# Performance work log

Measured on AMD Instinct MI355X. Metric: run time of the kernel, lower is better.

## Reference

```python
import jax, jax.numpy as jnp
import numpy as np

FLOW_ITERS = 8
DUAL_ITERS = 8
DUAL_STEP = 0.1
DUAL_MOM = 0.9
GRAPH_LAYERS = 2
BIG = 1e9


def _sparsemax(z, mask):
    # sparsemax along last axis; masked entries already hold -BIG, zeroed by mask after.
    V = z.shape[-1]
    zs = jnp.sort(z, axis=-1)[..., ::-1]
    cum = jnp.cumsum(zs, axis=-1)
    k = jnp.arange(1, V + 1, dtype=z.dtype)
    support = zs * k > (cum - 1.0)
    k_sel = jnp.sum(support.astype(jnp.int32), axis=-1, keepdims=True)
    tau = (jnp.take_along_axis(cum, k_sel - 1, axis=-1) - 1.0) / k_sel.astype(z.dtype)
    return jnp.maximum(z - tau, 0.0) * mask


def _min_cost_flow(props, demands):
    # iterative proportional flow routing: push relu(inflow - demand) along predicted proportions
    def body(flow, _):
        inflow = jnp.sum(flow, axis=1)[..., None]      # [B,V,1] inflow to each node
        adjusted = jax.nn.relu(inflow - demands)       # excess to re-route
        return props * adjusted, None                  # row i scaled by its excess
    flow0 = jnp.zeros_like(props)
    flow, _ = jax.lax.scan(body, flow0, None, length=FLOW_ITERS)
    return flow


def _dual_flow(dual_diff, adj):
    # Nesterov-momentum projected gradient on cost(x)=x^2 minus linear dual term, x>=0 on edges
    def body(carry, _):
        flow, acc = carry
        look = flow - DUAL_MOM * acc
        grad = 2.0 * look - dual_diff                  # d/dx x^2 - dual_diff
        acc = DUAL_MOM * acc + DUAL_STEP * grad
        flow = adj * jax.nn.relu(flow - acc)
        return (flow, acc), None
    z = jnp.zeros_like(dual_diff)
    (flow, _), _ = jax.lax.scan(body, (z, z), None, length=DUAL_ITERS)
    return flow


def setup_inputs():
    key = jax.random.key(0)
    ks = jax.random.split(key, 32)
    B, V, F, E, D, K, H = 8, 1200, 8, 16, 64, 2, 4
    node_features = jax.random.normal(ks[0], (B, V, F), dtype=jnp.float32)
    node_embeddings = jax.random.normal(ks[1], (B, V, E), dtype=jnp.float32)
    d = jax.random.normal(ks[2], (B, V, 1), dtype=jnp.float32)
    demands = d - jnp.mean(d, axis=1, keepdims=True)   # balanced supply/demand per graph
    eye = jnp.eye(V, dtype=jnp.float32)
    adj = (jax.random.uniform(ks[3], (B, V, V)) < (16.0 / V)).astype(jnp.float32) * (1.0 - eye)
    hop2 = jnp.clip(adj @ adj, 0.0, 1.0) * (1.0 - eye)
    neighborhoods = jnp.stack([adj, hop2], axis=0)     # [K,B,V,V] k-hop neighborhoods

    def dense(k, fin, fout):
        return (jax.random.normal(k, (fin, fout), dtype=jnp.float32) / np.sqrt(fin)).astype(jnp.float32)

    return dict(
        node_features=node_features, node_embeddings=node_embeddings,
        demands=demands, adj=adj, neighborhoods=neighborhoods,
        enc_w0=dense(ks[4], E + F, D), enc_b0=jnp.zeros((D,), jnp.float32),
        enc_w1=dense(ks[5], D, D), enc_b1=jnp.zeros((D,), jnp.float32),
        agg_w=(jax.random.normal(ks[6], (K, D, D)) / np.sqrt(D)).astype(jnp.float32),
        agg_b=jnp.zeros((K, D), jnp.float32),
        att_w=(jax.random.normal(ks[7], (H, D, D)) / np.sqrt(D)).astype(jnp.float32),
        att_b=jnp.zeros((H, D), jnp.float32),
        att_v=(jax.random.normal(ks[8], (H, D)) / np.sqrt(D)).astype(jnp.float32),
        gru_wu=dense(ks[9], 2 * D, D), gru_bu=jnp.zeros((D,), jnp.float32),
        gru_wr=dense(ks[10], 2 * D, D), gru_br=jnp.zeros((D,), jnp.float32),
        gru_wc=dense(ks[11], 2 * D, D), gru_bc=jnp.zeros((D,), jnp.float32),
        dec_w0=dense(ks[12], D, D), dec_b0=jnp.zeros((D,), jnp.float32),
        dec_w1=dense(ks[13], D, 1), dec_b1=jnp.zeros((1,), jnp.float32),
        dual_w0=dense(ks[14], D, D), dual_b0=jnp.zeros((D,), jnp.float32),
        dual_w1=dense(ks[15], D, 1), dual_b1=jnp.zeros((1,), jnp.float32),
    )


def reference(node_features, node_embeddings, demands, adj, neighborhoods,
              enc_w0, enc_b0, enc_w1, enc_b1, agg_w, agg_b, att_w, att_b, att_v,
              gru_wu, gru_bu, gru_wr, gru_br, gru_wc, gru_bc,
              dec_w0, dec_b0, dec_w1, dec_b1, dual_w0, dual_b0, dual_w1, dual_b1):
    H = att_w.shape[0]
    # node encoder MLP (tanh hidden, tanh final since activate_final=True)
    x = jnp.concatenate([node_embeddings, node_features], axis=-1)
    enc = jnp.tanh(jnp.tanh(x @ enc_w0 + enc_b0) @ enc_w1 + enc_b1)            # [B,V,D]

    deg = jnp.sum(neighborhoods, axis=-1, keepdims=True)
    nb_norm = neighborhoods / jnp.maximum(deg, 1.0)                            # [K,B,V,V]

    for _ in range(GRAPH_LAYERS):
        # per-hop neighborhood aggregation
        msg = jnp.einsum('kbuv,bvd->kbud', nb_norm, enc)
        agg = jnp.tanh(jnp.einsum('kbud,kde->kbue', msg, agg_w) + agg_b[:, None, None, :])
        # multi-head attention over the K hop levels
        proj = jnp.tanh(jnp.einsum('kbvd,hde->hkbve', agg, att_w) + att_b[:, None, None, None, :])
        scores = jnp.einsum('hkbve,he->hkbv', proj, att_v)
        attn = jax.nn.softmax(scores, axis=1)                                  # softmax over hops
        nxt = jnp.einsum('hkbv,kbvd->bvd', attn, agg) / H                      # mean over heads
        # GRU state update
        xs = jnp.concatenate([nxt, enc], axis=-1)
        u = jax.nn.sigmoid(xs @ gru_wu + gru_bu)
        r = jax.nn.sigmoid(xs @ gru_wr + gru_br)
        c = jnp.tanh(jnp.concatenate([nxt, r * enc], axis=-1) @ gru_wc + gru_bc)
        enc = u * enc + (1.0 - u) * c

    # primal: edge weights -> sparsemax -> min-cost-flow
    pred = (enc @ dec_w0 + dec_b0) @ dec_w1 + dec_b1                           # [B,V,1]
    pred_weights = adj * jnp.transpose(pred, (0, 2, 1))                        # [B,V,V]
    weights = -BIG * (1.0 - adj) + pred_weights
    flow_props = _sparsemax(weights, adj)
    flow = _min_cost_flow(flow_props, demands)
    flow_cost = jnp.sum(flow * flow, axis=(1, 2))                              # square cost

    # dual: potentials -> dual-diff -> dual flow solver
    dual = (enc @ dual_w0 + dual_b0) @ dual_w1 + dual_b1                       # [B,V,1]
    dual_diff = adj * (dual - jnp.transpose(dual, (0, 2, 1)))
    dflow = _dual_flow(dual_diff, adj)
    dual_demand = jnp.sum(dual * demands, axis=(1, 2))
    dual_cost = jnp.sum(dflow * dflow - dual_diff * dflow, axis=(1, 2)) - dual_demand

    return flow_cost - dual_cost                                               # duality-gap loss, [B]
```

## Files before the change

kernel.cpp:

```cpp
#include <hip/hip_runtime.h>

#define BB 8
#define VV 1200
#define DD 64
#define KH 2
#define NH 4
#define CAP 64
#define NB2CAP 384
#define NROW (BB*VV)
#define NKROW (KH*BB*VV)

__device__ __forceinline__ float wredsum(float v) {
#pragma unroll
  for (int o = 32; o > 0; o >>= 1) v += __shfl_xor(v, o, 64);
  return v;
}
__device__ __forceinline__ float gredsum(float v) {
#pragma unroll
  for (int o = 8; o > 0; o >>= 1) v += __shfl_xor(v, o, 64);
  return v;
}

__device__ __forceinline__ float tanh_f(float x) {
  float e = __expf(2.0f * x);
  return 1.0f - 2.0f / (e + 1.0f);
}
__device__ __forceinline__ float sigmoid_f(float x) { return 1.0f / (1.0f + __expf(-x)); }

__device__ __forceinline__ unsigned pack_bf16x2(float a, float b) {
  unsigned ua = __float_as_uint(a), ub = __float_as_uint(b);
  ua = (ua + 0x7fffu + ((ua >> 16) & 1u)) >> 16;
  ub = (ub + 0x7fffu + ((ub >> 16) & 1u)) & 0xffff0000u;
  return ua | ub;
}
__device__ __forceinline__ float bf_lo(unsigned u) { return __uint_as_float(u << 16); }
__device__ __forceinline__ float bf_hi(unsigned u) { return __uint_as_float(u & 0xffff0000u); }

__device__ __forceinline__ size_t nb_base(int row) {
  return (row < NROW) ? (size_t)row * CAP
                      : (size_t)NROW * CAP + (size_t)(row - NROW) * NB2CAP;
}

#define ENC2B (NROW / 64)
#define CSR2B (NKROW / 8)
__global__ void __launch_bounds__(512) k_pre(
    const float* __restrict__ nb, int* __restrict__ nb_cols, int* __restrict__ nb_cnt,
    const float* __restrict__ emb, const float* __restrict__ feat,
    const float* __restrict__ w0, const float* __restrict__ b0,
    const float* __restrict__ w1, const float* __restrict__ b1,
    unsigned* __restrict__ enc0,
    int* __restrict__ col_cnt, float* __restrict__ out, int out_size) {
  __shared__ float Xe[64][25];
  __shared__ float Ht[64][65];
  int bid = blockIdx.x;
  int tid = threadIdx.x;
  if (bid < ENC2B) {
    int tile0 = bid * 64;
    if (tid < 256) {
      int i = tid >> 2, f = tid & 3;
      float4 e4 = *(const float4*)(emb + (size_t)(tile0 + i) * 16 + f * 4);
      Xe[i][f * 4] = e4.x; Xe[i][f * 4 + 1] = e4.y; Xe[i][f * 4 + 2] = e4.z; Xe[i][f * 4 + 3] = e4.w;
    } else if (tid < 384) {
      int t = tid - 256; int i = t >> 1, f = t & 1;
      float4 f4 = *(const float4*)(feat + (size_t)(tile0 + i) * 8 + f * 4);
      Xe[i][16 + f * 4] = f4.x; Xe[i][16 + f * 4 + 1] = f4.y;
      Xe[i][16 + f * 4 + 2] = f4.z; Xe[i][16 + f * 4 + 3] = f4.w;
    }
    __syncthreads();
    int rsub = tid >> 4, cg = tid & 15;
    int c0 = cg * 4, r0 = rsub * 2;
    float a[2][4];
#pragma unroll
    for (int i = 0; i < 2; ++i)
#pragma unroll
      for (int j = 0; j < 4; ++j) a[i][j] = b0[c0 + j];
#pragma unroll
    for (int kk = 0; kk < 24; ++kk) {
      float4 w4 = *(const float4*)(w0 + kk * DD + c0);
      float x0 = Xe[r0][kk], x1 = Xe[r0 + 1][kk];
      a[0][0] = fmaf(x0, w4.x, a[0][0]); a[0][1] = fmaf(x0, w4.y, a[0][1]);
      a[0][2] = fmaf(x0, w4.z, a[0][2]); a[0][3] = fmaf(x0, w4.w, a[0][3]);
      a[1][0] = fmaf(x1, w4.x, a[1][0]); a[1][1] = fmaf(x1, w4.y, a[1][1]);
      a[1][2] = fmaf(x1, w4.z, a[1][2]); a[1][3] = fmaf(x1, w4.w, a[1][3]);
    }
#pragma unroll
    for (int i = 0; i < 2; ++i) {
      Ht[r0 + i][c0] = tanh_f(a[i][0]); Ht[r0 + i][c0 + 1] = tanh_f(a[i][1]);
      Ht[r0 + i][c0 + 2] = tanh_f(a[i][2]); Ht[r0 + i][c0 + 3] = tanh_f(a[i][3]);
    }
    __syncthreads();
    float g[2][4];
#pragma unroll
    for (int i = 0; i < 2; ++i)
#pragma unroll
      for (int j = 0; j < 4; ++j) g[i][j] = b1[c0 + j];
#pragma unroll 8
    for (int kk = 0; kk < DD; ++kk) {
      float4 w4 = *(const float4*)(w1 + kk * DD + c0);
      float x0 = Ht[r0][kk], x1 = Ht[r0 + 1][kk];
      g[0][0] = fmaf(x0, w4.x, g[0][0]); g[0][1] = fmaf(x0, w4.y, g[0][1]);
      g[0][2] = fmaf(x0, w4.z, g[0][2]); g[0][3] = fmaf(x0, w4.w, g[0][3]);
      g[1][0] = fmaf(x1, w4.x, g[1][0]); g[1][1] = fmaf(x1, w4.y, g[1][1]);
      g[1][2] = fmaf(x1, w4.z, g[1][2]); g[1][3] = fmaf(x1, w4.w, g[1][3]);
    }
#pragma unroll
    for (int i = 0; i < 2; ++i) {
      uint2 pk;
      pk.x = pack_bf16x2(tanh_f(g[i][0]), tanh_f(g[i][1]));
      pk.y = pack_bf16x2(tanh_f(g[i][2]), tanh_f(g[i][3]));
      ((uint2*)enc0)[(size_t)(tile0 + r0 + i) * 16 + cg] = pk;
    }
  } else if (bid < ENC2B + CSR2B) {
    int w = tid >> 6, lane = tid & 63;
    int row = (bid - ENC2B) * 8 + w;
    const float4* nb4 = (const float4*)(nb + (size_t)row * VV);
    float4 v[5];
#pragma unroll
    for (int c = 0; c < 4; ++c) v[c] = nb4[c * 64 + lane];
    v[4].x = v[4].y = v[4].z = v[4].w = 0.0f;
    if (lane < 44) v[4] = nb4[256 + lane];
    unsigned long long ltmask = (lane == 0) ? 0ull : ((1ull << lane) - 1ull);
    size_t base = nb_base(row);
    int cap = (row < NROW) ? CAP : NB2CAP;
    int off_base = 0;
#pragma unroll
    for (int c = 0; c < 5; ++c) {
      int nz0 = (v[c].x != 0.0f), nz1 = (v[c].y != 0.0f);
      int nz2 = (v[c].z != 0.0f), nz3 = (v[c].w != 0.0f);
      unsigned long long m0 = __ballot(nz0 != 0);
      unsigned long long m1 = __ballot(nz1 != 0);
      unsigned long long m2 = __ballot(nz2 != 0);
      unsigned long long m3 = __ballot(nz3 != 0);
      int lanepref = __popcll(m0 & ltmask) + __popcll(m1 & ltmask)
                   + __popcll(m2 & ltmask) + __popcll(m3 & ltmask);
      int chunkcnt = __popcll(m0) + __popcll(m1) + __popcll(m2) + __popcll(m3);
      int off = off_base + lanepref;
      int vi = (c * 64 + lane) * 4;
      if (nz0 && off < cap) nb_cols[base + off] = vi;
      off += nz0;
      if (nz1 && off < cap) nb_cols[base + off] = vi + 1;
      off += nz1;
      if (nz2 && off < cap) nb_cols[base + off] = vi + 2;
      off += nz2;
      if (nz3 && off < cap) nb_cols[base + off] = vi + 3;
      off_base += chunkcnt;
    }
    if (lane == 0) nb_cnt[row] = (off_base > cap) ? cap : off_base;
  } else {
    for (int i = tid; i < NROW; i += 512) col_cnt[i] = 0;
    if (tid < out_size) out[tid] = 0.0f;
  }
}

__global__ void __launch_bounds__(256) k_aggatt(
    const int* __restrict__ nb_cols, const int* __restrict__ nb_cnt,
    const unsigned* __restrict__ encIn,
    const float* __restrict__ agg_w, const float* __restrict__ agg_b,
    const float* __restrict__ att_w, const float* __restrict__ att_b,
    const float* __restrict__ att_v,
    float* __restrict__ agg, float* __restrict__ scores) {
  __shared__ float M[16][65];
  __shared__ float G[16][65];
  int tid = threadIdx.x;
  int tile0 = blockIdx.x * 16;
  int k = (tile0 >= NROW) ? 1 : 0;
  int bv0 = tile0 - k * NROW;
  int wid = tid >> 6, lane = tid & 63;
  int sub = lane >> 4, q = lane & 15;
  for (int ii = 0; ii < 4; ++ii) {
    int i = wid * 4 + ii;
    int row = tile0 + i;
    int bv = row - k * NROW;
    int b = bv / VV;
    const uint2* encU = (const uint2*)(encIn + (size_t)b * VV * 32);
    const int* cols = nb_cols + nb_base(row);
    int n = nb_cnt[row];
    float ax = 0.0f, ay = 0.0f, az = 0.0f, aw = 0.0f;
    int j = 0;
    int cc0 = 0, cc1 = 0, cc2 = 0, cc3 = 0;
    if (j + 16 <= n) {
      cc0 = cols[j + sub]; cc1 = cols[j + 4 + sub];
      cc2 = cols[j + 8 + sub]; cc3 = cols[j + 12 + sub];
    }
    while (j + 16 <= n) {
      int nj = j + 16;
      int p0 = 0, p1 = 0, p2 = 0, p3 = 0;
      if (nj + 16 <= n) {
        p0 = cols[nj + sub]; p1 = cols[nj + 4 + sub];
        p2 = cols[nj + 8 + sub]; p3 = cols[nj + 12 + sub];
      }
      uint2 u0 = encU[(size_t)cc0 * 16 + q];
      uint2 u1 = encU[(size_t)cc1 * 16 + q];
      uint2 u2 = encU[(size_t)cc2 * 16 + q];
      uint2 u3 = encU[(size_t)cc3 * 16 + q];
      ax += (bf_lo(u0.x) + bf_lo(u1.x)) + (bf_lo(u2.x) + bf_lo(u3.x));
      ay += (bf_hi(u0.x) + bf_hi(u1.x)) + (bf_hi(u2.x) + bf_hi(u3.x));
      az += (bf_lo(u0.y) + bf_lo(u1.y)) + (bf_lo(u2.y) + bf_lo(u3.y));
      aw += (bf_hi(u0.y) + bf_hi(u1.y)) + (bf_hi(u2.y) + bf_hi(u3.y));
      cc0 = p0; cc1 = p1; cc2 = p2; cc3 = p3;
      j = nj;
    }
    for (; j < n; j += 4) {
      int idx = j + sub;
      if (idx < n) {
        uint2 u = encU[(size_t)cols[idx] * 16 + q];
        ax += bf_lo(u.x); ay += bf_hi(u.x); az += bf_lo(u.y); aw += bf_hi(u.y);
      }
    }
#pragma unroll
    for (int o = 16; o < 64; o <<= 1) {
      ax += __shfl_xor(ax, o, 64);
      ay += __shfl_xor(ay, o, 64);
      az += __shfl_xor(az, o, 64);
      aw += __shfl_xor(aw, o, 64);
    }
    if (lane < 16) {
      float inv = 1.0f / fmaxf((float)n, 1.0f);
      M[i][q * 4] = ax * inv; M[i][q * 4 + 1] = ay * inv;
      M[i][q * 4 + 2] = az * inv; M[i][q * 4 + 3] = aw * inv;
    }
  }
  __syncthreads();
  int r = tid >> 4, cg = tid & 15;
  int c0 = cg * 4;
  const float* W = agg_w + (size_t)k * DD * DD;
  float acc[4];
#pragma unroll
  for (int j = 0; j < 4; ++j) acc[j] = agg_b[k * DD + c0 + j];
#pragma unroll 8
  for (int kk = 0; kk < DD; ++kk) {
    float4 w4 = *(const float4*)(W + kk * DD + c0);
    float x0 = M[r][kk];
    acc[0] = fmaf(x0, w4.x, acc[0]); acc[1] = fmaf(x0, w4.y, acc[1]);
    acc[2] = fmaf(x0, w4.z, acc[2]); acc[3] = fmaf(x0, w4.w, acc[3]);
  }
  float4 g4;
  g4.x = tanh_f(acc[0]); g4.y = tanh_f(acc[1]);
  g4.z = tanh_f(acc[2]); g4.w = tanh_f(acc[3]);
  G[r][c0] = g4.x; G[r][c0 + 1] = g4.y; G[r][c0 + 2] = g4.z; G[r][c0 + 3] = g4.w;
  *(float4*)(agg + (size_t)(tile0 + r) * DD + c0) = g4;
  __syncthreads();
#pragma unroll
  for (int h = 0; h < NH; ++h) {
    const float* Wh = att_w + (size_t)h * DD * DD;
    float a2[4];
#pragma unroll
    for (int j = 0; j < 4; ++j) a2[j] = att_b[h * DD + c0 + j];
#pragma unroll 8
    for (int kk = 0; kk < DD; ++kk) {
      float4 w4 = *(const float4*)(Wh + kk * DD + c0);
      float x0 = G[r][kk];
      a2[0] = fmaf(x0, w4.x, a2[0]); a2[1] = fmaf(x0, w4.y, a2[1]);
      a2[2] = fmaf(x0, w4.z, a2[2]); a2[3] = fmaf(x0, w4.w, a2[3]);
    }
    float4 v4 = *(const float4*)(att_v + h * DD + c0);
    float p = tanh_f(a2[0]) * v4.x + tanh_f(a2[1]) * v4.y
            + tanh_f(a2[2]) * v4.z + tanh_f(a2[3]) * v4.w;
    p = gredsum(p);
    if (cg == 0) scores[(size_t)(h * KH + k) * NROW + bv0 + r] = p;
  }
}

__global__ void __launch_bounds__(128) k_gru(
    const unsigned* __restrict__ encIn, const float* __restrict__ agg,
    const float* __restrict__ scores,
    const float* __restrict__ wu, const float* __restrict__ bu,
    const float* __restrict__ wr, const float* __restrict__ br,
    const float* __restrict__ wc, const float* __restrict__ bc,
    unsigned* __restrict__ encOut,
    int do_decode,
    const float* __restrict__ dw0, const float* __restrict__ db0,
    const float* __restrict__ dw1, const float* __restrict__ db1,
    const float* __restrict__ uw0, const float* __restrict__ ub0,
    const float* __restrict__ uw1, const float* __restrict__ ub1,
    float* __restrict__ pred, float* __restrict__ dualp) {
  __shared__ float X[16][129];
  __shared__ float EO[16][65];
  int tid = threadIdx.x;
  int tile0 = blockIdx.x * 16;
  int rsub = tid >> 4, cg = tid & 15;
  int c0 = cg * 4;
  int r0 = rsub * 2;
#pragma unroll
  for (int rep = 0; rep < 2; ++rep) {
    int idx = rep * 128 + tid; int i = idx >> 4, d4 = idx & 15;
    int row = tile0 + i;
    float W0 = 0.0f, W1 = 0.0f;
#pragma unroll
    for (int h = 0; h < NH; ++h) {
      float s0 = scores[(size_t)(h * KH + 0) * NROW + row];
      float s1 = scores[(size_t)(h * KH + 1) * NROW + row];
      float m = fmaxf(s0, s1);
      float e0 = __expf(s0 - m), e1 = __expf(s1 - m);
      float inv = 1.0f / (e0 + e1);
      W0 += e0 * inv; W1 += e1 * inv;
    }
    W0 *= 0.25f; W1 *= 0.25f;
    uint2 eu = ((const uint2*)encIn)[(size_t)row * 16 + d4];
    float4 a0 = *(const float4*)(agg + (size_t)row * DD + d4 * 4);
    float4 a1 = *(const float4*)(agg + (size_t)(NROW + row) * DD + d4 * 4);
    X[i][d4 * 4]     = W0 * a0.x + W1 * a1.x;
    X[i][d4 * 4 + 1] = W0 * a0.y + W1 * a1.y;
    X[i][d4 * 4 + 2] = W0 * a0.z + W1 * a1.z;
    X[i][d4 * 4 + 3] = W0 * a0.w + W1 * a1.w;
    X[i][64 + d4 * 4]     = bf_lo(eu.x);
    X[i][64 + d4 * 4 + 1] = bf_hi(eu.x);
    X[i][64 + d4 * 4 + 2] = bf_lo(eu.y);
    X[i][64 + d4 * 4 + 3] = bf_hi(eu.y);
  }
  __syncthreads();
  float au[2][4], ar[2][4];
#pragma unroll
  for (int i = 0; i < 2; ++i)
#pragma unroll
    for (int j = 0; j < 4; ++j) { au[i][j] = bu[c0 + j]; ar[i][j] = br[c0 + j]; }
#pragma unroll 4
  for (int kk = 0; kk < 2 * DD; ++kk) {
    float4 u4 = *(const float4*)(wu + kk * DD + c0);
    float4 r4 = *(const float4*)(wr + kk * DD + c0);
    float x0 = X[r0][kk], x1 = X[r0 + 1][kk];
    au[0][0] = fmaf(x0, u4.x, au[0][0]); au[0][1] = fmaf(x0, u4.y, au[0][1]);
    au[0][2] = fmaf(x0, u4.z, au[0][2]); au[0][3] = fmaf(x0, u4.w, au[0][3]);
    au[1][0] = fmaf(x1, u4.x, au[1][0]); au[1][1] = fmaf(x1, u4.y, au[1][1]);
    au[1][2] = fmaf(x1, u4.z, au[1][2]); au[1][3] = fmaf(x1, u4.w, au[1][3]);
    ar[0][0] = fmaf(x0, r4.x, ar[0][0]); ar[0][1] = fmaf(x0, r4.y, ar[0][1]);
    ar[0][2] = fmaf(x0, r4.z, ar[0][2]); ar[0][3] = fmaf(x0, r4.w, ar[0][3]);
    ar[1][0] = fmaf(x1, r4.x, ar[1][0]); ar[1][1] = fmaf(x1, r4.y, ar[1][1]);
    ar[1][2] = fmaf(x1, r4.z, ar[1][2]); ar[1][3] = fmaf(x1, r4.w, ar[1][3]);
  }
  float uu[2][4], encv[2][4];
#pragma unroll
  for (int i = 0; i < 2; ++i)
#pragma unroll
    for (int j = 0; j < 4; ++j) {
      uu[i][j] = sigmoid_f(au[i][j]);
      encv[i][j] = X[r0 + i][64 + c0 + j];
    }
  __syncthreads();
#pragma unroll
  for (int i = 0; i < 2; ++i)
#pragma unroll
    for (int j = 0; j < 4; ++j)
      X[r0 + i][64 + c0 + j] = encv[i][j] * sigmoid_f(ar[i][j]);
  __syncthreads();
  float ac[2][4];
#pragma unroll
  for (int i = 0; i < 2; ++i)
#pragma unroll
    for (int j = 0; j < 4; ++j) ac[i][j] = bc[c0 + j];
#pragma unroll 4
  for (int kk = 0; kk < 2 * DD; ++kk) {
    float4 c4 = *(const float4*)(wc + kk * DD + c0);
    float x0 = X[r0][kk], x1 = X[r0 + 1][kk];
    ac[0][0] = fmaf(x0, c4.x, ac[0][0]); ac[0][1] = fmaf(x0, c4.y, ac[0][1]);
    ac[0][2] = fmaf(x0, c4.z, ac[0][2]); ac[0][3] = fmaf(x0, c4.w, ac[0][3]);
    ac[1][0] = fmaf(x1, c4.x, ac[1][0]); ac[1][1] = fmaf(x1, c4.y, ac[1][1]);
    ac[1][2] = fmaf(x1, c4.z, ac[1][2]); ac[1][3] = fmaf(x1, c4.w, ac[1][3]);
  }
#pragma unroll
  for (int i = 0; i < 2; ++i) {
    float4 e4;
    e4.x = uu[i][0] * encv[i][0] + (1.0f - uu[i][0]) * tanh_f(ac[i][0]);
    e4.y = uu[i][1] * encv[i][1] + (1.0f - uu[i][1]) * tanh_f(ac[i][1]);
    e4.z = uu[i][2] * encv[i][2] + (1.0f - uu[i][2]) * tanh_f(ac[i][2]);
    e4.w = uu[i][3] * encv[i][3] + (1.0f - uu[i][3]) * tanh_f(ac[i][3]);
    uint2 pk; pk.x = pack_bf16x2(e4.x, e4.y); pk.y = pack_bf16x2(e4.z, e4.w);
    ((uint2*)encOut)[(size_t)(tile0 + r0 + i) * 16 + cg] = pk;
    EO[r0 + i][c0] = e4.x; EO[r0 + i][c0 + 1] = e4.y;
    EO[r0 + i][c0 + 2] = e4.z; EO[r0 + i][c0 + 3] = e4.w;
  }
  if (do_decode) {
    __syncthreads();
    float hd[2][4], hq[2][4];
#pragma unroll
    for (int i = 0; i < 2; ++i)
#pragma unroll
      for (int j = 0; j < 4; ++j) { hd[i][j] = db0[c0 + j]; hq[i][j] = ub0[c0 + j]; }
#pragma unroll 4
    for (int kk = 0; kk < DD; ++kk) {
      float4 d4 = *(const float4*)(dw0 + kk * DD + c0);
      float4 q4 = *(const float4*)(uw0 + kk * DD + c0);
      float x0 = EO[r0][kk], x1 = EO[r0 + 1][kk];
      hd[0][0] = fmaf(x0, d4.x, hd[0][0]); hd[0][1] = fmaf(x0, d4.y, hd[0][1]);
      hd[0][2] = fmaf(x0, d4.z, hd[0][2]); hd[0][3] = fmaf(x0, d4.w, hd[0][3]);
      hd[1][0] = fmaf(x1, d4.x, hd[1][0]); hd[1][1] = fmaf(x1, d4.y, hd[1][1]);
      hd[1][2] = fmaf(x1, d4.z, hd[1][2]); hd[1][3] = fmaf(x1, d4.w, hd[1][3]);
      hq[0][0] = fmaf(x0, q4.x, hq[0][0]); hq[0][1] = fmaf(x0, q4.y, hq[0][1]);
      hq[0][2] = fmaf(x0, q4.z, hq[0][2]); hq[0][3] = fmaf(x0, q4.w, hq[0][3]);
      hq[1][0] = fmaf(x1, q4.x, hq[1][0]); hq[1][1] = fmaf(x1, q4.y, hq[1][1]);
      hq[1][2] = fmaf(x1, q4.z, hq[1][2]); hq[1][3] = fmaf(x1, q4.w, hq[1][3]);
    }
    float4 dv = *(const float4*)(dw1 + c0);
    float4 qv = *(const float4*)(uw1 + c0);
#pragma unroll
    for (int i = 0; i < 2; ++i) {
      float p = hd[i][0] * dv.x + hd[i][1] * dv.y + hd[i][2] * dv.z + hd[i][3] * dv.w;
      float q = hq[i][0] * qv.x + hq[i][1] * qv.y + hq[i][2] * qv.z + hq[i][3] * qv.w;
      p = gredsum(p);
      q = gredsum(q);
      if (cg == 0) {
        pred[tile0 + r0 + i] = p + db1[0];
        dualp[tile0 + r0 + i] = q + ub1[0];
      }
    }
  }
}

__global__ void __launch_bounds__(256) k_primal_dual(
    const int* __restrict__ nb_cols, const int* __restrict__ nb_cnt,
    const float* __restrict__ pred, const float* __restrict__ dualp,
    const float* __restrict__ dem,
    float* __restrict__ rowsum,
    int* __restrict__ col_cnt, int* __restrict__ col_rows, float* __restrict__ col_vals,
    float* __restrict__ out) {
  __shared__ float bacc[BB];
  if (threadIdx.x < BB) bacc[threadIdx.x] = 0.0f;
  __syncthreads();
  int w = threadIdx.x >> 6, lane = threadIdx.x & 63;
  int row = blockIdx.x * 4 + w;
  int b = row / VV;
  int n = nb_cnt[row];
  int c = (lane < n) ? nb_cols[(size_t)row * CAP + lane] : 0;
  const float* predB = pred + (size_t)b * VV;
  const float* dualB = dualp + (size_t)b * VV;
  float z = (lane < n) ? predB[c] : -1e30f;
  float tau = 0.0f;
  if (n > 0) {
    bool in = (lane < n);
    for (int it = 0; it < 64; ++it) {
      float s = wredsum(in ? z : 0.0f);
      int cnt = (int)__popcll(__ballot(in));
      tau = (s - 1.0f) / (float)cnt;
      bool nin = (z > tau);
      if (__ballot(nin) == __ballot(in)) break;
      in = nin;
    }
  }
  float pv = (lane < n) ? fmaxf(z - tau, 0.0f) : 0.0f;
  float s2 = wredsum(pv * pv);
  if (lane == 0) rowsum[row] = s2;
  if (pv > 0.0f) {
    int g = b * VV + c;
    int j = atomicAdd(&col_cnt[g], 1);
    if (j < CAP) {
      col_rows[(size_t)g * CAP + j] = row - b * VV;
      col_vals[(size_t)g * CAP + j] = pv;
    }
  }
  float du = dualp[row];
  float es = 0.0f;
  if (lane < n) {
    float dd = du - dualB[c];
    float f = 0.0f, acm = 0.0f;
#pragma unroll
    for (int t = 0; t < 8; ++t) {
      float look = f - 0.9f * acm;
      float grad = 2.0f * look - dd;
      acm = 0.9f * acm + 0.1f * grad;
      f = fmaxf(f - acm, 0.0f);
    }
    es = f * f - dd * f;
  }
  float contrib = -es;
  if (lane == 0) contrib += du * dem[row];
  float ws_ = wredsum(contrib);
  if (lane == 0) atomicAdd(&bacc[b], ws_);
  __syncthreads();
  if (threadIdx.x < BB) {
    float t = bacc[threadIdx.x];
    if (t != 0.0f) atomicAdd(&out[threadIdx.x], t);
  }
}

__global__ void __launch_bounds__(1024) k_flow(
    const int* __restrict__ col_cnt, const int* __restrict__ col_rows,
    const float* __restrict__ col_vals, const float* __restrict__ dem,
    const float* __restrict__ rowsum, float* __restrict__ out) {
  __shared__ float aS[VV];
  __shared__ float red[16];
  int b = blockIdx.x;
  int tid = threadIdx.x;
  const float* demB = dem + (size_t)b * VV;
  for (int v = tid; v < VV; v += 1024) aS[v] = fmaxf(-demB[v], 0.0f);
  __syncthreads();
  for (int t = 0; t < 7; ++t) {
    float nv0 = 0.0f, nv1 = 0.0f;
    {
      int v = tid;
      if (v < VV) {
        int g = b * VV + v;
        int n = col_cnt[g]; if (n > CAP) n = CAP;
        const int* cr = col_rows + (size_t)g * CAP;
        const float* cv = col_vals + (size_t)g * CAP;
        float acc = 0.0f;
        for (int j = 0; j < n; ++j) acc += cv[j] * aS[cr[j]];
        nv0 = fmaxf(acc - demB[v], 0.0f);
      }
      v = tid + 1024;
      if (v < VV) {
        int g = b * VV + v;
        int n = col_cnt[g]; if (n > CAP) n = CAP;
        const int* cr = col_rows + (size_t)g * CAP;
        const float* cv = col_vals + (size_t)g * CAP;
        float acc = 0.0f;
        for (int j = 0; j < n; ++j) acc += cv[j] * aS[cr[j]];
        nv1 = fmaxf(acc - demB[v], 0.0f);
      }
    }
    __syncthreads();
    if (tid < VV) aS[tid] = nv0;
    if (tid + 1024 < VV) aS[tid + 1024] = nv1;
    __syncthreads();
  }
  float fc = 0.0f;
  for (int v = tid; v < VV; v += 1024) { float a = aS[v]; fc += a * a * rowsum[b * VV + v]; }
  fc = wredsum(fc);
  int wid = tid >> 6, lane = tid & 63;
  if (lane == 0) red[wid] = fc;
  __syncthreads();
  if (tid == 0) {
    float s = 0.0f;
#pragma unroll
    for (int i = 0; i < 16; ++i) s += red[i];
    atomicAdd(&out[b], s);
  }
}

extern "C" void kernel_launch(void* const* d_in, const int* in_sizes, int n_in,
                              void* d_out, int out_size, void* d_ws, size_t ws_size,
                              hipStream_t stream) {
  const float* feat   = (const float*)d_in[0];
  const float* emb    = (const float*)d_in[1];
  const float* dem    = (const float*)d_in[2];
  const float* nb     = (const float*)d_in[4];
  const float* enc_w0 = (const float*)d_in[5];
  const float* enc_b0 = (const float*)d_in[6];
  const float* enc_w1 = (const float*)d_in[7];
  const float* enc_b1 = (const float*)d_in[8];
  const float* agg_w  = (const float*)d_in[9];
  const float* agg_b  = (const float*)d_in[10];
  const float* att_w  = (const float*)d_in[11];
  const float* att_b  = (const float*)d_in[12];
  const float* att_v  = (const float*)d_in[13];
  const float* gru_wu = (const float*)d_in[14];
  const float* gru_bu = (const float*)d_in[15];
  const float* gru_wr = (const float*)d_in[16];
  const float* gru_br = (const float*)d_in[17];
  const float* gru_wc = (const float*)d_in[18];
  const float* gru_bc = (const float*)d_in[19];
  const float* dec_w0 = (const float*)d_in[20];
  const float* dec_b0 = (const float*)d_in[21];
  const float* dec_w1 = (const float*)d_in[22];
  const float* dec_b1 = (const float*)d_in[23];
  const float* dual_w0= (const float*)d_in[24];
  const float* dual_b0= (const float*)d_in[25];
  const float* dual_w1= (const float*)d_in[26];
  const float* dual_b1= (const float*)d_in[27];
  float* out = (float*)d_out;

  unsigned* enc0 = (unsigned*)d_ws;
  unsigned* enc1 = enc0 + (size_t)NROW * 32;
  float* aggbuf   = (float*)(enc1 + (size_t)NROW * 32);
  float* scores   = aggbuf + (size_t)NKROW * DD;
  float* pred     = scores + (size_t)NH * KH * NROW;
  float* dualp    = pred + NROW;
  float* rowsum   = dualp + NROW;
  float* col_vals = rowsum + NROW;
  int* col_cnt  = (int*)(col_vals + (size_t)NROW * CAP);
  int* nb_cnt   = col_cnt + NROW;
  int* col_rows = nb_cnt + NKROW;
  int* nb_cols  = col_rows + (size_t)NROW * CAP;

  (void)in_sizes; (void)n_in; (void)ws_size;

  k_pre<<<ENC2B + CSR2B + 1, 512, 0, stream>>>(
      nb, nb_cols, nb_cnt, emb, feat, enc_w0, enc_b0, enc_w1, enc_b1, enc0,
      col_cnt, out, out_size);

  const unsigned* encIn = enc0;
  unsigned* encOut = enc1;
  for (int l = 0; l < 2; ++l) {
    k_aggatt<<<NKROW / 16, 256, 0, stream>>>(nb_cols, nb_cnt, encIn,
                                             agg_w, agg_b, att_w, att_b, att_v,
                                             aggbuf, scores);
    k_gru<<<NROW / 16, 128, 0, stream>>>(encIn, aggbuf, scores,
                                         gru_wu, gru_bu, gru_wr, gru_br, gru_wc, gru_bc,
                                         encOut,
                                         (l == 1) ? 1 : 0,
                                         dec_w0, dec_b0, dec_w1, dec_b1,
                                         dual_w0, dual_b0, dual_w1, dual_b1, pred, dualp);
    const unsigned* t = encIn; encIn = encOut; encOut = (unsigned*)t;
  }

  k_primal_dual<<<NROW / 4, 256, 0, stream>>>(nb_cols, nb_cnt, pred, dualp, dem,
                                              rowsum, col_cnt, col_rows, col_vals, out);
  k_flow<<<BB, 1024, 0, stream>>>(col_cnt, col_rows, col_vals, dem, rowsum, out);
}
```

Measured before the change: 544.2 us.

## Split neighbor gather from MLP and retile dense matmuls to 4x2 per thread

Measured after the change: 506.2 us. -7.0%, faster.

```diff
diff --git a/kernel.cpp b/kernel.cpp
--- a/kernel.cpp
+++ b/kernel.cpp
@@ -15,9 +15,9 @@
   for (int o = 32; o > 0; o >>= 1) v += __shfl_xor(v, o, 64);
   return v;
 }
-__device__ __forceinline__ float gredsum(float v) {
-#pragma unroll
-  for (int o = 8; o > 0; o >>= 1) v += __shfl_xor(v, o, 64);
+__device__ __forceinline__ float gredsum32(float v) {
+#pragma unroll
+  for (int o = 16; o > 0; o >>= 1) v += __shfl_xor(v, o, 64);
   return v;
 }
 
@@ -152,112 +152,132 @@
   }
 }
 
-__global__ void __launch_bounds__(256) k_aggatt(
+__global__ void __launch_bounds__(256) k_gather(
     const int* __restrict__ nb_cols, const int* __restrict__ nb_cnt,
-    const unsigned* __restrict__ encIn,
+    const unsigned* __restrict__ encIn, float* __restrict__ msg) {
+  int w = threadIdx.x >> 6, lane = threadIdx.x & 63;
+  int row = blockIdx.x * 4 + w;
+  int k = (row >= NROW) ? 1 : 0;
+  int bv = row - k * NROW;
+  int b = bv / VV;
+  const uint2* encU = (const uint2*)(encIn + (size_t)b * VV * 32);
+  const int* cols = nb_cols + nb_base(row);
+  int n = nb_cnt[row];
+  int sub = lane >> 4, q = lane & 15;
+  float ax = 0.0f, ay = 0.0f, az = 0.0f, aw = 0.0f;
+  int j = 0;
+  int cc0 = 0, cc1 = 0, cc2 = 0, cc3 = 0;
+  if (j + 16 <= n) {
+    cc0 = cols[j + sub]; cc1 = cols[j + 4 + sub];
+    cc2 = cols[j + 8 + sub]; cc3 = cols[j + 12 + sub];
+  }
+  while (j + 16 <= n) {
+    int nj = j + 16;
+    int p0 = 0, p1 = 0, p2 = 0, p3 = 0;
+    if (nj + 16 <= n) {
+      p0 = cols[nj + sub]; p1 = cols[nj + 4 + sub];
+      p2 = cols[nj + 8 + sub]; p3 = cols[nj + 12 + sub];
+    }
+    uint2 u0 = encU[(size_t)cc0 * 16 + q];
+    uint2 u1 = encU[(size_t)cc1 * 16 + q];
+    uint2 u2 = encU[(size_t)cc2 * 16 + q];
+    uint2 u3 = encU[(size_t)cc3 * 16 + q];
+    ax += (bf_lo(u0.x) + bf_lo(u1.x)) + (bf_lo(u2.x) + bf_lo(u3.x));
+    ay += (bf_hi(u0.x) + bf_hi(u1.x)) + (bf_hi(u2.x) + bf_hi(u3.x));
+    az += (bf_lo(u0.y) + bf_lo(u1.y)) + (bf_lo(u2.y) + bf_lo(u3.y));
+    aw += (bf_hi(u0.y) + bf_hi(u1.y)) + (bf_hi(u2.y) + bf_hi(u3.y));
+    cc0 = p0; cc1 = p1; cc2 = p2; cc3 = p3;
+    j = nj;
+  }
+  for (; j < n; j += 4) {
+    int idx = j + sub;
+    if (idx < n) {
+      uint2 u = encU[(size_t)cols[idx] * 16 + q];
+      ax += bf_lo(u.x); ay += bf_hi(u.x); az += bf_lo(u.y); aw += bf_hi(u.y);
+    }
+  }
+#pragma unroll
+  for (int o = 16; o < 64; o <<= 1) {
+    ax += __shfl_xor(ax, o, 64);
+    ay += __shfl_xor(ay, o, 64);
+    az += __shfl_xor(az, o, 64);
+    aw += __shfl_xor(aw, o, 64);
+  }
+  if (lane < 16) {
+    float inv = 1.0f / fmaxf((float)n, 1.0f);
+    float4 r; r.x = ax * inv; r.y = ay * inv; r.z = az * inv; r.w = aw * inv;
+    ((float4*)(msg + (size_t)row * DD))[q] = r;
+  }
+}
+
+__global__ void __launch_bounds__(512) k_mlp(
+    const float* __restrict__ msg,
     const float* __restrict__ agg_w, const float* __restrict__ agg_b,
     const float* __restrict__ att_w, const float* __restrict__ att_b,
     const float* __restrict__ att_v,
     float* __restrict__ agg, float* __restrict__ scores) {
-  __shared__ float M[16][65];
-  __shared__ float G[16][65];
+  __shared__ float M[64][65];
+  __shared__ float G[64][65];
   int tid = threadIdx.x;
-  int tile0 = blockIdx.x * 16;
+  int tile0 = blockIdx.x * 64;
   int k = (tile0 >= NROW) ? 1 : 0;
   int bv0 = tile0 - k * NROW;
-  int wid = tid >> 6, lane = tid & 63;
-  int sub = lane >> 4, q = lane & 15;
-  for (int ii = 0; ii < 4; ++ii) {
-    int i = wid * 4 + ii;
-    int row = tile0 + i;
-    int bv = row - k * NROW;
-    int b = bv / VV;
-    const uint2* encU = (const uint2*)(encIn + (size_t)b * VV * 32);
-    const int* cols = nb_cols + nb_base(row);
-    int n = nb_cnt[row];
-    float ax = 0.0f, ay = 0.0f, az = 0.0f, aw = 0.0f;
-    int j = 0;
-    int cc0 = 0, cc1 = 0, cc2 = 0, cc3 = 0;
-    if (j + 16 <= n) {
-      cc0 = cols[j + sub]; cc1 = cols[j + 4 + sub];
-      cc2 = cols[j + 8 + sub]; cc3 = cols[j + 12 + sub];
-    }
-    while (j + 16 <= n) {
-      int nj = j + 16;
-      int p0 = 0, p1 = 0, p2 = 0, p3 = 0;
-      if (nj + 16 <= n) {
-        p0 = cols[nj + sub]; p1 = cols[nj + 4 + sub];
-        p2 = cols[nj + 8 + sub]; p3 = cols[nj + 12 + sub];
-      }
-      uint2 u0 = encU[(size_t)cc0 * 16 + q];
-      uint2 u1 = encU[(size_t)cc1 * 16 + q];
-      uint2 u2 = encU[(size_t)cc2 * 16 + q];
-      uint2 u3 = encU[(size_t)cc3 * 16 + q];
-      ax += (bf_lo(u0.x) + bf_lo(u1.x)) + (bf_lo(u2.x) + bf_lo(u3.x));
-      ay += (bf_hi(u0.x) + bf_hi(u1.x)) + (bf_hi(u2.x) + bf_hi(u3.x));
-      az += (bf_lo(u0.y) + bf_lo(u1.y)) + (bf_lo(u2.y) + bf_lo(u3.y));
-      aw += (bf_hi(u0.y) + bf_hi(u1.y)) + (bf_hi(u2.y) + bf_hi(u3.y));
-      cc0 = p0; cc1 = p1; cc2 = p2; cc3 = p3;
-      j = nj;
-    }
-    for (; j < n; j += 4) {
-      int idx = j + sub;
-      if (idx < n) {
-        uint2 u = encU[(size_t)cols[idx] * 16 + q];
-        ax += bf_lo(u.x); ay += bf_hi(u.x); az += bf_lo(u.y); aw += bf_hi(u.y);
-      }
-    }
-#pragma unroll
-    for (int o = 16; o < 64; o <<= 1) {
-      ax += __shfl_xor(ax, o, 64);
-      ay += __shfl_xor(ay, o, 64);
-      az += __shfl_xor(az, o, 64);
-      aw += __shfl_xor(aw, o, 64);
-    }
-    if (lane < 16) {
-      float inv = 1.0f / fmaxf((float)n, 1.0f);
-      M[i][q * 4] = ax * inv; M[i][q * 4 + 1] = ay * inv;
-      M[i][q * 4 + 2] = az * inv; M[i][q * 4 + 3] = aw * inv;
-    }
-  }
-  __syncthreads();
-  int r = tid >> 4, cg = tid & 15;
-  int c0 = cg * 4;
+  int strip = tid >> 5, cg2 = tid & 31;
+  int c0 = cg2 * 2;
+  int r0 = strip * 4;
+#pragma unroll
+  for (int rep = 0; rep < 2; ++rep) {
+    int idx = rep * 512 + tid; int i = idx >> 4, d4 = idx & 15;
+    float4 m4 = *(const float4*)(msg + (size_t)(tile0 + i) * DD + d4 * 4);
+    M[i][d4 * 4] = m4.x; M[i][d4 * 4 + 1] = m4.y; M[i][d4 * 4 + 2] = m4.z; M[i][d4 * 4 + 3] = m4.w;
+  }
+  __syncthreads();
   const float* W = agg_w + (size_t)k * DD * DD;
-  float acc[4];
-#pragma unroll
-  for (int j = 0; j < 4; ++j) acc[j] = agg_b[k * DD + c0 + j];
+  float acc[4][2];
+#pragma unroll
+  for (int i = 0; i < 4; ++i) {
+    acc[i][0] = agg_b[k * DD + c0]; acc[i][1] = agg_b[k * DD + c0 + 1];
+  }
 #pragma unroll 8
   for (int kk = 0; kk < DD; ++kk) {
-    float4 w4 = *(const float4*)(W + kk * DD + c0);
-    float x0 = M[r][kk];
-    acc[0] = fmaf(x0, w4.x, acc[0]); acc[1] = fmaf(x0, w4.y, acc[1]);
-    acc[2] = fmaf(x0, w4.z, acc[2]); acc[3] = fmaf(x0, w4.w, acc[3]);
-  }
-  float4 g4;
-  g4.x = tanh_f(acc[0]); g4.y = tanh_f(acc[1]);
-  g4.z = tanh_f(acc[2]); g4.w = tanh_f(acc[3]);
-  G[r][c0] = g4.x; G[r][c0 + 1] = g4.y; G[r][c0 + 2] = g4.z; G[r][c0 + 3] = g4.w;
-  *(float4*)(agg + (size_t)(tile0 + r) * DD + c0) = g4;
+    float2 w2 = *(const float2*)(W + kk * DD + c0);
+#pragma unroll
+    for (int i = 0; i < 4; ++i) {
+      float x = M[r0 + i][kk];
+      acc[i][0] = fmaf(x, w2.x, acc[i][0]); acc[i][1] = fmaf(x, w2.y, acc[i][1]);
+    }
+  }
+#pragma unroll
+  for (int i = 0; i < 4; ++i) {
+    float g0 = tanh_f(acc[i][0]), g1 = tanh_f(acc[i][1]);
+    G[r0 + i][c0] = g0; G[r0 + i][c0 + 1] = g1;
+    *(float2*)(agg + (size_t)(tile0 + r0 + i) * DD + c0) = make_float2(g0, g1);
+  }
   __syncthreads();
 #pragma unroll
   for (int h = 0; h < NH; ++h) {
     const float* Wh = att_w + (size_t)h * DD * DD;
-    float a2[4];
-#pragma unroll
-    for (int j = 0; j < 4; ++j) a2[j] = att_b[h * DD + c0 + j];
+    float a2[4][2];
+#pragma unroll
+    for (int i = 0; i < 4; ++i) {
+      a2[i][0] = att_b[h * DD + c0]; a2[i][1] = att_b[h * DD + c0 + 1];
+    }
 #pragma unroll 8
     for (int kk = 0; kk < DD; ++kk) {
-      float4 w4 = *(const float4*)(Wh + kk * DD + c0);
-      float x0 = G[r][kk];
-      a2[0] = fmaf(x0, w4.x, a2[0]); a2[1] = fmaf(x0, w4.y, a2[1]);
-      a2[2] = fmaf(x0, w4.z, a2[2]); a2[3] = fmaf(x0, w4.w, a2[3]);
-    }
-    float4 v4 = *(const float4*)(att_v + h * DD + c0);
-    float p = tanh_f(a2[0]) * v4.x + tanh_f(a2[1]) * v4.y
-            + tanh_f(a2[2]) * v4.z + tanh_f(a2[3]) * v4.w;
-    p = gredsum(p);
-    if (cg == 0) scores[(size_t)(h * KH + k) * NROW + bv0 + r] = p;
+      float2 w2 = *(const float2*)(Wh + kk * DD + c0);
+#pragma unroll
+      for (int i = 0; i < 4; ++i) {
+        float x = G[r0 + i][kk];
+        a2[i][0] = fmaf(x, w2.x, a2[i][0]); a2[i][1] = fmaf(x, w2.y, a2[i][1]);
+      }
+    }
+    float2 v2 = *(const float2*)(att_v + h * DD + c0);
+#pragma unroll
+    for (int i = 0; i < 4; ++i) {
+      float p = tanh_f(a2[i][0]) * v2.x + tanh_f(a2[i][1]) * v2.y;
+      p = gredsum32(p);
+      if (cg2 == 0) scores[(size_t)(h * KH + k) * NROW + bv0 + r0 + i] = p;
+    }
   }
 }
 
@@ -278,9 +298,9 @@
   __shared__ float EO[16][65];
   int tid = threadIdx.x;
   int tile0 = blockIdx.x * 16;
-  int rsub = tid >> 4, cg = tid & 15;
-  int c0 = cg * 4;
-  int r0 = rsub * 2;
+  int strip = tid >> 5, cg2 = tid & 31;
+  int c0 = cg2 * 2;
+  int r0 = strip * 4;
 #pragma unroll
   for (int rep = 0; rep < 2; ++rep) {
     int idx = rep * 128 + tid; int i = idx >> 4, d4 = idx & 15;
@@ -309,96 +329,83 @@
     X[i][64 + d4 * 4 + 3] = bf_hi(eu.y);
   }
   __syncthreads();
-  float au[2][4], ar[2][4];
-#pragma unroll
-  for (int i = 0; i < 2; ++i)
-#pragma unroll
-    for (int j = 0; j < 4; ++j) { au[i][j] = bu[c0 + j]; ar[i][j] = br[c0 + j]; }
-#pragma unroll 4
+  float au[4][2], ar[4][2];
+#pragma unroll
+  for (int i = 0; i < 4; ++i) {
+    au[i][0] = bu[c0]; au[i][1] = bu[c0 + 1];
+    ar[i][0] = br[c0]; ar[i][1] = br[c0 + 1];
+  }
+#pragma unroll 8
   for (int kk = 0; kk < 2 * DD; ++kk) {
-    float4 u4 = *(const float4*)(wu + kk * DD + c0);
-    float4 r4 = *(const float4*)(wr + kk * DD + c0);
-    float x0 = X[r0][kk], x1 = X[r0 + 1][kk];
-    au[0][0] = fmaf(x0, u4.x, au[0][0]); au[0][1] = fmaf(x0, u4.y, au[0][1]);
-    au[0][2] = fmaf(x0, u4.z, au[0][2]); au[0][3] = fmaf(x0, u4.w, au[0][3]);
-    au[1][0] = fmaf(x1, u4.x, au[1][0]); au[1][1] = fmaf(x1, u4.y, au[1][1]);
-    au[1][2] = fmaf(x1, u4.z, au[1][2]); au[1][3] = fmaf(x1, u4.w, au[1][3]);
-    ar[0][0] = fmaf(x0, r4.x, ar[0][0]); ar[0][1] = fmaf(x0, r4.y, ar[0][1]);
-    ar[0][2] = fmaf(x0, r4.z, ar[0][2]); ar[0][3] = fmaf(x0, r4.w, ar[0][3]);
-    ar[1][0] = fmaf(x1, r4.x, ar[1][0]); ar[1][1] = fmaf(x1, r4.y, ar[1][1]);
-    ar[1][2] = fmaf(x1, r4.z, ar[1][2]); ar[1][3] = fmaf(x1, r4.w, ar[1][3]);
-  }
-  float uu[2][4], encv[2][4];
-#pragma unroll
-  for (int i = 0; i < 2; ++i)
-#pragma unroll
-    for (int j = 0; j < 4; ++j) {
-      uu[i][j] = sigmoid_f(au[i][j]);
-      encv[i][j] = X[r0 + i][64 + c0 + j];
-    }
-  __syncthreads();
-#pragma unroll
-  for (int i = 0; i < 2; ++i)
-#pragma unroll
-    for (int j = 0; j < 4; ++j)
-      X[r0 + i][64 + c0 + j] = encv[i][j] * sigmoid_f(ar[i][j]);
-  __syncthreads();
-  float ac[2][4];
-#pragma unroll
-  for (int i = 0; i < 2; ++i)
-#pragma unroll
-    for (int j = 0; j < 4; ++j) ac[i][j] = bc[c0 + j];
-#pragma unroll 4
+    float2 u2 = *(const float2*)(wu + kk * DD + c0);
+    float2 r2 = *(const float2*)(wr + kk * DD + c0);
+#pragma unroll
+    for (int i = 0; i < 4; ++i) {
+      float x = X[r0 + i][kk];
+      au[i][0] = fmaf(x, u2.x, au[i][0]); au[i][1] = fmaf(x, u2.y, au[i][1]);
+      ar[i][0] = fmaf(x, r2.x, ar[i][0]); ar[i][1] = fmaf(x, r2.y, ar[i][1]);
+    }
+  }
+  float uu[4][2], encv[4][2];
+#pragma unroll
+  for (int i = 0; i < 4; ++i) {
+    uu[i][0] = sigmoid_f(au[i][0]); uu[i][1] = sigmoid_f(au[i][1]);
+    encv[i][0] = X[r0 + i][64 + c0]; encv[i][1] = X[r0 + i][64 + c0 + 1];
+  }
+  __syncthreads();
+#pragma unroll
+  for (int i = 0; i < 4; ++i) {
+    X[r0 + i][64 + c0]     = encv[i][0] * sigmoid_f(ar[i][0]);
+    X[r0 + i][64 + c0 + 1] = encv[i][1] * sigmoid_f(ar[i][1]);
+  }
+  __syncthreads();
+  float ac[4][2];
+#pragma unroll
+  for (int i = 0; i < 4; ++i) { ac[i][0] = bc[c0]; ac[i][1] = bc[c0 + 1]; }
+#pragma unroll 8
   for (int kk = 0; kk < 2 * DD; ++kk) {
-    float4 c4 = *(const float4*)(wc + kk * DD + c0);
-    float x0 = X[r0][kk], x1 = X[r0 + 1][kk];
-    ac[0][0] = fmaf(x0, c4.x, ac[0][0]); ac[0][1] = fmaf(x0, c4.y, ac[0][1]);
-    ac[0][2] = fmaf(x0, c4.z, ac[0][2]); ac[0][3] = fmaf(x0, c4.w, ac[0][3]);
-    ac[1][0] = fmaf(x1, c4.x, ac[1][0]); ac[1][1] = fmaf(x1, c4.y, ac[1][1]);
-    ac[1][2] = fmaf(x1, c4.z, ac[1][2]); ac[1][3] = fmaf(x1, c4.w, ac[1][3]);
-  }
-#pragma unroll
-  for (int i = 0; i < 2; ++i) {
-    float4 e4;
-    e4.x = uu[i][0] * encv[i][0] + (1.0f - uu[i][0]) * tanh_f(ac[i][0]);
-    e4.y = uu[i][1] * encv[i][1] + (1.0f - uu[i][1]) * tanh_f(ac[i][1]);
-    e4.z = uu[i][2] * encv[i][2] + (1.0f - uu[i][2]) * tanh_f(ac[i][2]);
-    e4.w = uu[i][3] * encv[i][3] + (1.0f - uu[i][3]) * tanh_f(ac[i][3]);
-    uint2 pk; pk.x = pack_bf16x2(e4.x, e4.y); pk.y = pack_bf16x2(e4.z, e4.w);
-    ((uint2*)encOut)[(size_t)(tile0 + r0 + i) * 16 + cg] = pk;
-    EO[r0 + i][c0] = e4.x; EO[r0 + i][c0 + 1] = e4.y;
-    EO[r0 + i][c0 + 2] = e4.z; EO[r0 + i][c0 + 3] = e4.w;
+    float2 c2 = *(const float2*)(wc + kk * DD + c0);
+#pragma unroll
+    for (int i = 0; i < 4; ++i) {
+      float x = X[r0 + i][kk];
+      ac[i][0] = fmaf(x, c2.x, ac[i][0]); ac[i][1] = fmaf(x, c2.y, ac[i][1]);
+    }
+  }
+#pragma unroll
+  for (int i = 0; i < 4; ++i) {
+    float e0 = uu[i][0] * encv[i][0] + (1.0f - uu[i][0]) * tanh_f(ac[i][0]);
+    float e1 = uu[i][1] * encv[i][1] + (1.0f - uu[i][1]) * tanh_f(ac[i][1]);
+    ((unsigned*)encOut)[(size_t)(tile0 + r0 + i) * 32 + cg2] = pack_bf16x2(e0, e1);
+    EO[r0 + i][c0] = e0; EO[r0 + i][c0 + 1] = e1;
   }
   if (do_decode) {
     __syncthreads();
-    float hd[2][4], hq[2][4];
-#pragma unroll
-    for (int i = 0; i < 2; ++i)
-#pragma unroll
-      for (int j = 0; j < 4; ++j) { hd[i][j] = db0[c0 + j]; hq[i][j] = ub0[c0 + j]; }
-#pragma unroll 4
+    float hd[4][2], hq[4][2];
+#pragma unroll
+    for (int i = 0; i < 4; ++i) {
+      hd[i][0] = db0[c0]; hd[i][1] = db0[c0 + 1];
+      hq[i][0] = ub0[c0]; hq[i][1] = ub0[c0 + 1];
+    }
+#pragma unroll 8
     for (int kk = 0; kk < DD; ++kk) {
-      float4 d4 = *(const float4*)(dw0 + kk * DD + c0);
-      float4 q4 = *(const float4*)(uw0 + kk * DD + c0);
-      float x0 = EO[r0][kk], x1 = EO[r0 + 1][kk];
-      hd[0][0] = fmaf(x0, d4.x, hd[0][0]); hd[0][1] = fmaf(x0, d4.y, hd[0][1]);
-      hd[0][2] = fmaf(x0, d4.z, hd[0][2]); hd[0][3] = fmaf(x0, d4.w, hd[0][3]);
-      hd[1][0] = fmaf(x1, d4.x, hd[1][0]); hd[1][1] = fmaf(x1, d4.y, hd[1][1]);
-      hd[1][2] = fmaf(x1, d4.z, hd[1][2]); hd[1][3] = fmaf(x1, d4.w, hd[1][3]);
-      hq[0][0] = fmaf(x0, q4.x, hq[0][0]); hq[0][1] = fmaf(x0, q4.y, hq[0][1]);
-      hq[0][2] = fmaf(x0, q4.z, hq[0][2]); hq[0][3] = fmaf(x0, q4.w, hq[0][3]);
-      hq[1][0] = fmaf(x1, q4.x, hq[1][0]); hq[1][1] = fmaf(x1, q4.y, hq[1][1]);
-      hq[1][2] = fmaf(x1, q4.z, hq[1][2]); hq[1][3] = fmaf(x1, q4.w, hq[1][3]);
-    }
-    float4 dv = *(const float4*)(dw1 + c0);
-    float4 qv = *(const float4*)(uw1 + c0);
-#pragma unroll
-    for (int i = 0; i < 2; ++i) {
-      float p = hd[i][0] * dv.x + hd[i][1] * dv.y + hd[i][2] * dv.z + hd[i][3] * dv.w;
-      float q = hq[i][0] * qv.x + hq[i][1] * qv.y + hq[i][2] * qv.z + hq[i][3] * qv.w;
-      p = gredsum(p);
-      q = gredsum(q);
-      if (cg == 0) {
+      float2 d2 = *(const float2*)(dw0 + kk * DD + c0);
+      float2 q2 = *(const float2*)(uw0 + kk * DD + c0);
+#pragma unroll
+      for (int i = 0; i < 4; ++i) {
+        float x = EO[r0 + i][kk];
+        hd[i][0] = fmaf(x, d2.x, hd[i][0]); hd[i][1] = fmaf(x, d2.y, hd[i][1]);
+        hq[i][0] = fmaf(x, q2.x, hq[i][0]); hq[i][1] = fmaf(x, q2.y, hq[i][1]);
+      }
+    }
+    float2 dv = *(const float2*)(dw1 + c0);
+    float2 qv = *(const float2*)(uw1 + c0);
+#pragma unroll
+    for (int i = 0; i < 4; ++i) {
+      float p = hd[i][0] * dv.x + hd[i][1] * dv.y;
+      float q = hq[i][0] * qv.x + hq[i][1] * qv.y;
+      p = gredsum32(p);
+      q = gredsum32(q);
+      if (cg2 == 0) {
         pred[tile0 + r0 + i] = p + db1[0];
         dualp[tile0 + r0 + i] = q + ub1[0];
       }
@@ -560,7 +567,8 @@
 
   unsigned* enc0 = (unsigned*)d_ws;
   unsigned* enc1 = enc0 + (size_t)NROW * 32;
-  float* aggbuf   = (float*)(enc1 + (size_t)NROW * 32);
+  float* msg      = (float*)(enc1 + (size_t)NROW * 32);
+  float* aggbuf   = msg + (size_t)NKROW * DD;
   float* scores   = aggbuf + (size_t)NKROW * DD;
   float* pred     = scores + (size_t)NH * KH * NROW;
   float* dualp    = pred + NROW;
@@ -580,9 +588,9 @@
   const unsigned* encIn = enc0;
   unsigned* encOut = enc1;
   for (int l = 0; l < 2; ++l) {
-    k_aggatt<<<NKROW / 16, 256, 0, stream>>>(nb_cols, nb_cnt, encIn,
-                                             agg_w, agg_b, att_w, att_b, att_v,
-                                             aggbuf, scores);
+    k_gather<<<NKROW / 4, 256, 0, stream>>>(nb_cols, nb_cnt, encIn, msg);
+    k_mlp<<<NKROW / 64, 512, 0, stream>>>(msg, agg_w, agg_b, att_w, att_b, att_v,
+                                          aggbuf, scores);
     k_gru<<<NROW / 16, 128, 0, stream>>>(encIn, aggbuf, scores,
                                          gru_wu, gru_bu, gru_wr, gru_br, gru_wc, gru_bc,
                                          encOut,
```
